# Kernel optimization log

Hardware: AMD Instinct MI355X
Metric: run time of the kernel (lower is better)

Reference implementation:

```python
import jax, jax.numpy as jnp
import numpy as np

OUTPUT_SIZE = 7
STRIDES = (4, 8, 16, 32)
IMG = 1024.0


def setup_inputs() -> dict:
    key = jax.random.key(0)
    ks = jax.random.split(key, 7)
    B, C, N = 2, 256, 1000
    p2 = jax.random.normal(ks[0], (B, 256, 256, C), jnp.float32)
    p3 = jax.random.normal(ks[1], (B, 128, 128, C), jnp.float32)
    p4 = jax.random.normal(ks[2], (B, 64, 64, C), jnp.float32)
    p5 = jax.random.normal(ks[3], (B, 32, 32, C), jnp.float32)
    # box sizes log-uniform in [16, 800] px so all pyramid levels get RoIs
    wh = jnp.exp(jax.random.uniform(ks[4], (N, 2), minval=jnp.log(16.0), maxval=jnp.log(800.0)))
    cxy = jax.random.uniform(ks[5], (N, 2), minval=0.0, maxval=IMG)
    x1y1 = jnp.clip(cxy - wh / 2.0, 0.0, IMG - 1.0)
    x2y2 = jnp.clip(cxy + wh / 2.0, x1y1 + 1.0, IMG - 1.0)
    rois = jnp.concatenate([x1y1, x2y2], axis=1)  # [N,4] = [x1,y1,x2,y2]
    batch_indices = jax.random.randint(ks[6], (N,), 0, B, dtype=jnp.int32)
    return {"p2": p2, "p3": p3, "p4": p4, "p5": p5, "rois": rois, "batch_indices": batch_indices}


def _crop_and_resize(fm, boxes, box_idx, crop):
    """tf.image.crop_and_resize (bilinear, extrapolation_value=0).
    fm: [B,H,W,C]; boxes: [N,4] normalized [y1,x1,y2,x2]; box_idx: [N] int.
    Returns [N, crop, crop, C]."""
    H, W = fm.shape[1], fm.shape[2]
    y1, x1, y2, x2 = boxes[:, 0], boxes[:, 1], boxes[:, 2], boxes[:, 3]
    g = jnp.arange(crop, dtype=fm.dtype) / (crop - 1)  # crop > 1
    in_y = (y1[:, None] + (y2 - y1)[:, None] * g) * (H - 1)  # [N,crop]
    in_x = (x1[:, None] + (x2 - x1)[:, None] * g) * (W - 1)  # [N,crop]
    valid_y = (in_y >= 0) & (in_y <= H - 1)
    valid_x = (in_x >= 0) & (in_x <= W - 1)
    y0 = jnp.floor(in_y); x0 = jnp.floor(in_x)
    ly = in_y - y0; lx = in_x - x0
    y0i = jnp.clip(y0, 0, H - 1).astype(jnp.int32)
    y1i = jnp.clip(jnp.ceil(in_y), 0, H - 1).astype(jnp.int32)
    x0i = jnp.clip(x0, 0, W - 1).astype(jnp.int32)
    x1i = jnp.clip(jnp.ceil(in_x), 0, W - 1).astype(jnp.int32)
    b = box_idx[:, None, None]
    tl = fm[b, y0i[:, :, None], x0i[:, None, :]]  # [N,crop,crop,C]
    tr = fm[b, y0i[:, :, None], x1i[:, None, :]]
    bl = fm[b, y1i[:, :, None], x0i[:, None, :]]
    br = fm[b, y1i[:, :, None], x1i[:, None, :]]
    lxe = lx[:, None, :, None]
    top = tl + (tr - tl) * lxe
    bot = bl + (br - bl) * lxe
    out = top + (bot - top) * ly[:, :, None, None]
    mask = (valid_y[:, :, None] & valid_x[:, None, :])[..., None]
    return jnp.where(mask, out, jnp.zeros((), fm.dtype))


def reference(p2, p3, p4, p5, rois, batch_indices):
    fms = (p2, p3, p4, p5)
    w = rois[:, 2] - rois[:, 0]
    h = rois[:, 3] - rois[:, 1]
    levels = jnp.log(jnp.sqrt(h * w) / 224.0) / jnp.log(2.0) + 4.0
    levels = jnp.clip(jnp.round(levels).astype(jnp.int32), 2, 5)  # [N]
    N = rois.shape[0]
    C = p2.shape[-1]
    c = OUTPUT_SIZE
    out = jnp.zeros((N, c, c, C), p2.dtype)
    for i, stride in enumerate(STRIDES):
        fm = fms[i]
        H, W = fm.shape[1], fm.shape[2]
        bx = rois / float(stride)
        # normalized [y1, x1, y2, x2]
        boxes = jnp.stack([bx[:, 1] / H, bx[:, 0] / W, bx[:, 3] / H, bx[:, 2] / W], axis=1)
        feats = _crop_and_resize(fm, boxes, batch_indices, c)
        mask = (levels == i + 2)[:, None, None, None]
        out = jnp.where(mask, feats, out)
    # boolean-mask + concat + argsort-restore in the original is an identity
    # reordering: result i comes from roi i's assigned level; batch indices
    # are restored to the original order.
    return out, batch_indices
```

## Files before the change

kernel.cpp:

```cpp
#include <hip/hip_runtime.h>
#include <math.h>

#define NCH  256
#define CROP 7

__device__ __forceinline__ float lerpf(float a, float b, float t) {
    return a + (b - a) * t;
}

__global__ __launch_bounds__(256) void roialign_fpn_kernel(
    const float* __restrict__ p2, const float* __restrict__ p3,
    const float* __restrict__ p4, const float* __restrict__ p5,
    const float* __restrict__ rois, const int* __restrict__ bidx,
    float* __restrict__ out)
{
    const int tid = threadIdx.x;
    const int cv  = tid & 63;
    const int pl  = tid >> 6;
    const int pix = blockIdx.x * 4 + pl;
    const int n   = blockIdx.y;
    if (pix >= CROP * CROP) return;
    const int jy = pix / CROP;
    const int jx = pix - jy * CROP;

    const float rx1 = rois[4*n+0];
    const float ry1 = rois[4*n+1];
    const float rx2 = rois[4*n+2];
    const float ry2 = rois[4*n+3];
    const float w = rx2 - rx1;
    const float h = ry2 - ry1;

    const float lvlf = logf(sqrtf(h * w) / 224.0f) / logf(2.0f) + 4.0f;
    int lvl = (int)rintf(lvlf);
    lvl = lvl < 2 ? 2 : (lvl > 5 ? 5 : lvl);
    const int i = lvl - 2;

    const int H = 256 >> i;
    const float* fm = (i == 0) ? p2 : (i == 1) ? p3 : (i == 2) ? p4 : p5;
    const float inv = 1.0f / (float)((4 << i) * H);
    const float Hm1 = (float)(H - 1);

    const float gy = (float)jy / 6.0f;
    const float gx = (float)jx / 6.0f;
    const float ny1 = ry1 * inv, ny2 = ry2 * inv;
    const float nx1 = rx1 * inv, nx2 = rx2 * inv;
    const float in_y = (ny1 + (ny2 - ny1) * gy) * Hm1;
    const float in_x = (nx1 + (nx2 - nx1) * gx) * Hm1;

    const bool valid = (in_y >= 0.0f) && (in_y <= Hm1) &&
                       (in_x >= 0.0f) && (in_x <= Hm1);

    const float y0f = floorf(in_y);
    const float x0f = floorf(in_x);
    const float ly = in_y - y0f;
    const float lx = in_x - x0f;
    const int y0 = (int)fminf(fmaxf(y0f,          0.0f), Hm1);
    const int y1 = (int)fminf(fmaxf(ceilf(in_y),  0.0f), Hm1);
    const int x0 = (int)fminf(fmaxf(x0f,          0.0f), Hm1);
    const int x1 = (int)fminf(fmaxf(ceilf(in_x),  0.0f), Hm1);

    const int b = bidx[n];
    const size_t row0 = ((size_t)b * H + y0) * (size_t)H;
    const size_t row1 = ((size_t)b * H + y1) * (size_t)H;
    const int c = cv * 4;

    const float4 tl = *(const float4*)(fm + (row0 + x0) * NCH + c);
    const float4 tr = *(const float4*)(fm + (row0 + x1) * NCH + c);
    const float4 bl = *(const float4*)(fm + (row1 + x0) * NCH + c);
    const float4 br = *(const float4*)(fm + (row1 + x1) * NCH + c);

    float4 r;
    r.x = lerpf(lerpf(tl.x, tr.x, lx), lerpf(bl.x, br.x, lx), ly);
    r.y = lerpf(lerpf(tl.y, tr.y, lx), lerpf(bl.y, br.y, lx), ly);
    r.z = lerpf(lerpf(tl.z, tr.z, lx), lerpf(bl.z, br.z, lx), ly);
    r.w = lerpf(lerpf(tl.w, tr.w, lx), lerpf(bl.w, br.w, lx), ly);
    if (!valid) { r.x = 0.0f; r.y = 0.0f; r.z = 0.0f; r.w = 0.0f; }

    *(float4*)(out + ((size_t)n * (CROP * CROP) + pix) * NCH + c) = r;
}

__global__ void bidx_copy_kernel(const int* __restrict__ bidx,
                                 float* __restrict__ out_tail, int N)
{
    const int g = blockIdx.x * blockDim.x + threadIdx.x;
    if (g < N) out_tail[g] = (float)bidx[g];
}

extern "C" void kernel_launch(void* const* d_in, const int* in_sizes, int n_in,
                              void* d_out, int out_size, void* d_ws, size_t ws_size,
                              hipStream_t stream) {
    const float* p2   = (const float*)d_in[0];
    const float* p3   = (const float*)d_in[1];
    const float* p4   = (const float*)d_in[2];
    const float* p5   = (const float*)d_in[3];
    const float* rois = (const float*)d_in[4];
    const int*   bidx = (const int*)d_in[5];
    float* out = (float*)d_out;

    const int N = in_sizes[5];

    dim3 grid((CROP * CROP + 3) / 4, N);
    roialign_fpn_kernel<<<grid, 256, 0, stream>>>(p2, p3, p4, p5, rois, bidx, out);

    float* tail = out + (size_t)N * (CROP * CROP * NCH);
    bidx_copy_kernel<<<(N + 255) / 256, 256, 0, stream>>>(bidx, tail, N);
}
```

Measured before the change: 225.3 us.

## Fuse batch-index copy into RoIAlign kernel and loop pixels per block

The separate batch-index copy kernel is folded into the main kernel, so one launch does both jobs. Each block now covers about half of a RoI's 49 output pixels in a loop, giving 2 blocks per RoI instead of 13, and per-RoI setup (level selection, batch base) is shared across iterations. Output writes use nontemporal stores so the output stream does not evict cache lines. The trade-off is fewer, longer blocks, which lowers parallelism and may hide memory latency less well.

```diff
diff --git a/kernel.cpp b/kernel.cpp
--- a/kernel.cpp
+++ b/kernel.cpp
@@ -3,6 +3,9 @@
 
 #define NCH  256
 #define CROP 7
+#define NPIX 49
+
+typedef float vf4 __attribute__((ext_vector_type(4)));
 
 __device__ __forceinline__ float lerpf(float a, float b, float t) {
     return a + (b - a) * t;
@@ -12,16 +15,13 @@
     const float* __restrict__ p2, const float* __restrict__ p3,
     const float* __restrict__ p4, const float* __restrict__ p5,
     const float* __restrict__ rois, const int* __restrict__ bidx,
-    float* __restrict__ out)
+    float* __restrict__ out, float* __restrict__ out_tail)
 {
-    const int tid = threadIdx.x;
-    const int cv  = tid & 63;
-    const int pl  = tid >> 6;
-    const int pix = blockIdx.x * 4 + pl;
-    const int n   = blockIdx.y;
-    if (pix >= CROP * CROP) return;
-    const int jy = pix / CROP;
-    const int jx = pix - jy * CROP;
+    const int tid  = threadIdx.x;
+    const int cv   = tid & 63;
+    const int pl   = tid >> 6;
+    const int half = blockIdx.x;
+    const int n    = blockIdx.y;
 
     const float rx1 = rois[4*n+0];
     const float ry1 = rois[4*n+1];
@@ -40,50 +40,59 @@
     const float inv = 1.0f / (float)((4 << i) * H);
     const float Hm1 = (float)(H - 1);
 
-    const float gy = (float)jy / 6.0f;
-    const float gx = (float)jx / 6.0f;
+    const int b = bidx[n];
+    if (half == 0 && tid == 0) out_tail[n] = (float)b;
+
     const float ny1 = ry1 * inv, ny2 = ry2 * inv;
     const float nx1 = rx1 * inv, nx2 = rx2 * inv;
-    const float in_y = (ny1 + (ny2 - ny1) * gy) * Hm1;
-    const float in_x = (nx1 + (nx2 - nx1) * gx) * Hm1;
+    const size_t bbase = (size_t)b * H * H;
 
-    const bool valid = (in_y >= 0.0f) && (in_y <= Hm1) &&
-                       (in_x >= 0.0f) && (in_x <= Hm1);
+    const int c = cv * 4;
+    float* outp = out + (size_t)n * (NPIX * NCH) + c;
 
-    const float y0f = floorf(in_y);
-    const float x0f = floorf(in_x);
-    const float ly = in_y - y0f;
-    const float lx = in_x - x0f;
-    const int y0 = (int)fminf(fmaxf(y0f,          0.0f), Hm1);
-    const int y1 = (int)fminf(fmaxf(ceilf(in_y),  0.0f), Hm1);
-    const int x0 = (int)fminf(fmaxf(x0f,          0.0f), Hm1);
-    const int x1 = (int)fminf(fmaxf(ceilf(in_x),  0.0f), Hm1);
+    const int pix0  = half * 28;
+    const int iters = half ? 6 : 7;
 
-    const int b = bidx[n];
-    const size_t row0 = ((size_t)b * H + y0) * (size_t)H;
-    const size_t row1 = ((size_t)b * H + y1) * (size_t)H;
-    const int c = cv * 4;
+    for (int it = 0; it < iters; ++it) {
+        const int pix = pix0 + it * 4 + pl;
+        if (pix >= NPIX) continue;
 
-    const float4 tl = *(const float4*)(fm + (row0 + x0) * NCH + c);
-    const float4 tr = *(const float4*)(fm + (row0 + x1) * NCH + c);
-    const float4 bl = *(const float4*)(fm + (row1 + x0) * NCH + c);
-    const float4 br = *(const float4*)(fm + (row1 + x1) * NCH + c);
+        const int jy = pix / CROP;
+        const int jx = pix - jy * CROP;
+        const float gy = (float)jy / 6.0f;
+        const float gx = (float)jx / 6.0f;
+        const float in_y = (ny1 + (ny2 - ny1) * gy) * Hm1;
+        const float in_x = (nx1 + (nx2 - nx1) * gx) * Hm1;
 
-    float4 r;
-    r.x = lerpf(lerpf(tl.x, tr.x, lx), lerpf(bl.x, br.x, lx), ly);
-    r.y = lerpf(lerpf(tl.y, tr.y, lx), lerpf(bl.y, br.y, lx), ly);
-    r.z = lerpf(lerpf(tl.z, tr.z, lx), lerpf(bl.z, br.z, lx), ly);
-    r.w = lerpf(lerpf(tl.w, tr.w, lx), lerpf(bl.w, br.w, lx), ly);
-    if (!valid) { r.x = 0.0f; r.y = 0.0f; r.z = 0.0f; r.w = 0.0f; }
+        const bool valid = (in_y >= 0.0f) && (in_y <= Hm1) &&
+                           (in_x >= 0.0f) && (in_x <= Hm1);
 
-    *(float4*)(out + ((size_t)n * (CROP * CROP) + pix) * NCH + c) = r;
-}
+        const float y0f = floorf(in_y);
+        const float x0f = floorf(in_x);
+        const float ly = in_y - y0f;
+        const float lx = in_x - x0f;
+        const int y0 = (int)fminf(fmaxf(y0f,         0.0f), Hm1);
+        const int y1 = (int)fminf(fmaxf(ceilf(in_y), 0.0f), Hm1);
+        const int x0 = (int)fminf(fmaxf(x0f,         0.0f), Hm1);
+        const int x1 = (int)fminf(fmaxf(ceilf(in_x), 0.0f), Hm1);
 
-__global__ void bidx_copy_kernel(const int* __restrict__ bidx,
-                                 float* __restrict__ out_tail, int N)
-{
-    const int g = blockIdx.x * blockDim.x + threadIdx.x;
-    if (g < N) out_tail[g] = (float)bidx[g];
+        const size_t row0 = bbase + (size_t)y0 * H;
+        const size_t row1 = bbase + (size_t)y1 * H;
+
+        const vf4 tl = *(const vf4*)(fm + (row0 + x0) * NCH + c);
+        const vf4 tr = *(const vf4*)(fm + (row0 + x1) * NCH + c);
+        const vf4 bl = *(const vf4*)(fm + (row1 + x0) * NCH + c);
+        const vf4 br = *(const vf4*)(fm + (row1 + x1) * NCH + c);
+
+        vf4 r;
+        r.x = lerpf(lerpf(tl.x, tr.x, lx), lerpf(bl.x, br.x, lx), ly);
+        r.y = lerpf(lerpf(tl.y, tr.y, lx), lerpf(bl.y, br.y, lx), ly);
+        r.z = lerpf(lerpf(tl.z, tr.z, lx), lerpf(bl.z, br.z, lx), ly);
+        r.w = lerpf(lerpf(tl.w, tr.w, lx), lerpf(bl.w, br.w, lx), ly);
+        if (!valid) { r.x = 0.0f; r.y = 0.0f; r.z = 0.0f; r.w = 0.0f; }
+
+        __builtin_nontemporal_store(r, (vf4*)(outp + (size_t)pix * NCH));
+    }
 }
 
 extern "C" void kernel_launch(void* const* d_in, const int* in_sizes, int n_in,
@@ -98,10 +107,9 @@
     float* out = (float*)d_out;
 
     const int N = in_sizes[5];
+    float* tail = out + (size_t)N * (NPIX * NCH);
 
-    dim3 grid((CROP * CROP + 3) / 4, N);
-    roialign_fpn_kernel<<<grid, 256, 0, stream>>>(p2, p3, p4, p5, rois, bidx, out);
-
-    float* tail = out + (size_t)N * (CROP * CROP * NCH);
-    bidx_copy_kernel<<<(N + 255) / 256, 256, 0, stream>>>(bidx, tail, N);
+    dim3 grid(2, N);
+    roialign_fpn_kernel<<<grid, 256, 0, stream>>>(p2, p3, p4, p5, rois, bidx,
+                                                  out, tail);
 }
```

Result: no change. 228.9 us (+1.6%).
